# Performance work log

Hardware: AMD Instinct MI355X
Metric: run time of the kernel (lower is better)

Reference implementation:

```python
import jax, jax.numpy as jnp
import numpy as np
import math

EPS = 1e-6
MAX_NORM = 1.0 - 1e-3


def _clip_to_ball(x):
    # Keep point strictly inside the unit ball (||x|| < 1).
    norm = jnp.maximum(jnp.linalg.norm(x, axis=-1, keepdims=True), EPS)
    factor = jnp.minimum(MAX_NORM / norm, 1.0)
    return x * factor


def setup_inputs() -> dict:
    key = jax.random.key(0)
    k1, k2 = jax.random.split(key)
    B, C, D = 8192, 4096, 512
    euclidean_emb = jax.random.normal(k1, (B, D), dtype=jnp.float32)
    centroids = jax.random.uniform(k2, (C, D), dtype=jnp.float32, minval=-0.01, maxval=0.01)
    log_c = jnp.asarray(math.log(1.0), dtype=jnp.float32)
    return {"euclidean_emb": euclidean_emb, "log_c": log_c, "centroids": centroids}


def reference(euclidean_emb, log_c, centroids):
    # torch code used c = self.log_c.exp().item() -> c is detached scalar
    c = jax.lax.stop_gradient(jnp.exp(log_c))
    sqrt_c = jnp.sqrt(c)

    # expmap0: Euclidean -> Poincare ball
    v_norm = jnp.maximum(jnp.linalg.norm(euclidean_emb, axis=-1, keepdims=True), EPS)
    coeff = jnp.tanh(sqrt_c * v_norm) / (sqrt_c * v_norm)
    x_h = _clip_to_ball(coeff * euclidean_emb)   # (B, D)
    cen_h = _clip_to_ball(centroids)             # (C, D)

    # Pairwise Poincare distance via GEMM (same math as the expanded (B,C,D) form):
    # ||x - y||^2 = ||x||^2 + ||y||^2 - 2 <x, y>
    x2_raw = jnp.sum(x_h * x_h, axis=-1)         # (B,)
    y2_raw = jnp.sum(cen_h * cen_h, axis=-1)     # (C,)
    x2 = jnp.minimum(x2_raw, MAX_NORM ** 2)
    y2 = jnp.minimum(y2_raw, MAX_NORM ** 2)
    xy = x_h @ cen_h.T                           # (B, C) GEMM
    diff2 = x2_raw[:, None] + y2_raw[None, :] - 2.0 * xy

    denom = jnp.maximum((1.0 - c * x2)[:, None] * (1.0 - c * y2)[None, :], EPS)
    arg = jnp.maximum(1.0 + c * (2.0 * diff2) / denom, 1.0 + EPS)
    dists = jnp.arccosh(arg) / sqrt_c            # (B, C)
    return dists, x_h, cen_h
```

## Files before the change

### kernel.cpp

```cpp
#include <hip/hip_runtime.h>
#include <math.h>

#define EPSV 1e-6f
#define MAX_NORM (1.0f - 1e-3f)

typedef __attribute__((ext_vector_type(8))) short short8;
typedef __attribute__((ext_vector_type(4))) float f32x4;

__device__ inline ushort f32_to_bf16(float f) {
    union { float f; uint32_t u; } cv;
    cv.f = f;
    uint32_t u = cv.u;
    u += 0x7FFFu + ((u >> 16) & 1u);
    return (ushort)(u >> 16);
}

__device__ inline void glds16(const ushort* gsrc, ushort* ldsdst) {
    auto* g = (const __attribute__((address_space(1))) uint32_t*)gsrc;
    auto* l = (__attribute__((address_space(3))) uint32_t*)ldsdst;
    __builtin_amdgcn_global_load_lds(g, l, 16, 0, 0);
}

__device__ inline short8 ds_read128(const ushort* p) {
    auto* l3 = (const __attribute__((address_space(3))) ushort*)p;
    const uint32_t addr = (uint32_t)(uintptr_t)l3;
    short8 v;
    asm volatile("ds_read_b128 %0, %1" : "=&v"(v) : "v"(addr));
    return v;
}

__global__ void rows_emb_kernel(const float* __restrict__ emb,
                                const float* __restrict__ logc,
                                float* __restrict__ xh,
                                ushort* __restrict__ xbf,
                                float* __restrict__ x2raw,
                                float* __restrict__ dxv) {
    const int D = 512;
    const int row = blockIdx.x;
    const int lane = threadIdx.x;

    const float4* r4 = (const float4*)(emb + (size_t)row * D);
    float4 a = r4[2 * lane];
    float4 b = r4[2 * lane + 1];

    float ss = a.x * a.x + a.y * a.y + a.z * a.z + a.w * a.w
             + b.x * b.x + b.y * b.y + b.z * b.z + b.w * b.w;
#pragma unroll
    for (int off = 32; off > 0; off >>= 1) ss += __shfl_xor(ss, off, 64);

    const float c  = expf(logc[0]);
    const float sc = sqrtf(c);

    const float tn    = sqrtf(ss);
    const float vn    = fmaxf(tn, EPSV);
    const float coeff = tanhf(sc * vn) / (sc * vn);
    const float pre   = coeff * tn;
    const float fac   = fminf(MAX_NORM / fmaxf(pre, EPSV), 1.0f);
    const float scale = coeff * fac;

    float4 oa, ob;
    oa.x = a.x * scale; oa.y = a.y * scale; oa.z = a.z * scale; oa.w = a.w * scale;
    ob.x = b.x * scale; ob.y = b.y * scale; ob.z = b.z * scale; ob.w = b.w * scale;

    float4* o4 = (float4*)(xh + (size_t)row * D);
    o4[2 * lane]     = oa;
    o4[2 * lane + 1] = ob;

    union { ushort u[8]; uint4 v; } pk;
    pk.u[0] = f32_to_bf16(oa.x); pk.u[1] = f32_to_bf16(oa.y);
    pk.u[2] = f32_to_bf16(oa.z); pk.u[3] = f32_to_bf16(oa.w);
    pk.u[4] = f32_to_bf16(ob.x); pk.u[5] = f32_to_bf16(ob.y);
    pk.u[6] = f32_to_bf16(ob.z); pk.u[7] = f32_to_bf16(ob.w);
    ((uint4*)(xbf + (size_t)row * D))[lane] = pk.v;

    if (lane == 0) {
        const float sq = scale * scale * ss;
        x2raw[row] = sq;
        dxv[row]   = 1.0f - c * fminf(sq, MAX_NORM * MAX_NORM);
    }
}

__global__ void rows_cen_kernel(const float* __restrict__ cen,
                                const float* __restrict__ logc,
                                float* __restrict__ ch,
                                ushort* __restrict__ cbf,
                                float* __restrict__ y2raw,
                                float* __restrict__ dyv) {
    const int D = 512;
    const int row = blockIdx.x;
    const int lane = threadIdx.x;

    const float4* r4 = (const float4*)(cen + (size_t)row * D);
    float4 a = r4[2 * lane];
    float4 b = r4[2 * lane + 1];

    float ss = a.x * a.x + a.y * a.y + a.z * a.z + a.w * a.w
             + b.x * b.x + b.y * b.y + b.z * b.z + b.w * b.w;
#pragma unroll
    for (int off = 32; off > 0; off >>= 1) ss += __shfl_xor(ss, off, 64);

    const float c = expf(logc[0]);

    const float tn    = sqrtf(ss);
    const float scale = fminf(MAX_NORM / fmaxf(tn, EPSV), 1.0f);

    float4 oa, ob;
    oa.x = a.x * scale; oa.y = a.y * scale; oa.z = a.z * scale; oa.w = a.w * scale;
    ob.x = b.x * scale; ob.y = b.y * scale; ob.z = b.z * scale; ob.w = b.w * scale;

    float4* o4 = (float4*)(ch + (size_t)row * D);
    o4[2 * lane]     = oa;
    o4[2 * lane + 1] = ob;

    union { ushort u[8]; uint4 v; } pk;
    pk.u[0] = f32_to_bf16(oa.x); pk.u[1] = f32_to_bf16(oa.y);
    pk.u[2] = f32_to_bf16(oa.z); pk.u[3] = f32_to_bf16(oa.w);
    pk.u[4] = f32_to_bf16(ob.x); pk.u[5] = f32_to_bf16(ob.y);
    pk.u[6] = f32_to_bf16(ob.z); pk.u[7] = f32_to_bf16(ob.w);
    ((uint4*)(cbf + (size_t)row * D))[lane] = pk.v;

    if (lane == 0) {
        const float sq = scale * scale * ss;
        y2raw[row] = sq;
        dyv[row]   = 1.0f - c * fminf(sq, MAX_NORM * MAX_NORM);
    }
}

#define BM 256
#define BN 256
#define BKT 32
#define EPST 68

__global__ __launch_bounds__(512, 2)
void gemm_epi_kernel(const ushort* __restrict__ Abf,
                     const ushort* __restrict__ Bbf,
                     const float* __restrict__ x2raw,
                     const float* __restrict__ dxv,
                     const float* __restrict__ y2raw,
                     const float* __restrict__ dyv,
                     const float* __restrict__ logc,
                     float* __restrict__ out,
                     int M, int N, int K) {
    __shared__ __align__(16) char smem[65536];

    const int tid  = threadIdx.x;
    const int lane = tid & 63;
    const int wid  = tid >> 6;
    const int wm   = wid >> 2;
    const int wn   = wid & 3;

    const int bm = blockIdx.y;
    const int bn = blockIdx.x;

    const ushort* Ab = Abf + (size_t)bm * BM * K;
    const ushort* Bb = Bbf + (size_t)bn * BN * K;

    f32x4 acc[8][4];
#pragma unroll
    for (int m = 0; m < 8; m++)
#pragma unroll
        for (int n = 0; n < 4; n++) acc[m][n] = (f32x4){0.f, 0.f, 0.f, 0.f};

    const size_t fragoff = (size_t)(lane & 15) * K + ((lane >> 4) * 8);

    auto Asb = [&](int p) { return (ushort*)(smem + p * 16384); };
    auto Bsb = [&](int p) { return (ushort*)(smem + 32768 + p * 16384); };

    auto stage = [&](int p, int k0) {
#pragma unroll
        for (int j = 0; j < 2; j++) {
            const int s = wid * 2 + j;
            const size_t goff = (size_t)(s * 16) * K + k0 + fragoff;
            glds16(Ab + goff, Asb(p) + s * 512);
            glds16(Bb + goff, Bsb(p) + s * 512);
        }
    };

    stage(0, 0);
    stage(1, BKT);
    asm volatile("s_waitcnt vmcnt(4)" ::: "memory");
    __builtin_amdgcn_s_barrier();

    const int NT = K / BKT;
    int p = 0;
    for (int t = 0; t < NT; t++) {
        short8 af[8], bfr[4];
#pragma unroll
        for (int n = 0; n < 4; n++)
            bfr[n] = ds_read128(Bsb(p) + (wn * 4 + n) * 512 + lane * 8);
        af[0] = ds_read128(Asb(p) + (wm * 8 + 0) * 512 + lane * 8);
        af[1] = ds_read128(Asb(p) + (wm * 8 + 1) * 512 + lane * 8);

#pragma unroll
        for (int q = 0; q < 4; q++) {
            if (q < 3) {
                af[2 * q + 2] = ds_read128(Asb(p) + (wm * 8 + 2 * q + 2) * 512 + lane * 8);
                af[2 * q + 3] = ds_read128(Asb(p) + (wm * 8 + 2 * q + 3) * 512 + lane * 8);
                asm volatile("s_waitcnt lgkmcnt(2)" ::: "memory");
            } else {
                asm volatile("s_waitcnt lgkmcnt(0)" ::: "memory");
            }
            __builtin_amdgcn_sched_barrier(0);
            __builtin_amdgcn_s_setprio(1);
#pragma unroll
            for (int mm = 0; mm < 2; mm++)
#pragma unroll
                for (int n = 0; n < 4; n++)
                    acc[2 * q + mm][n] = __builtin_amdgcn_mfma_f32_16x16x32_bf16(
                        af[2 * q + mm], bfr[n], acc[2 * q + mm][n], 0, 0, 0);
            __builtin_amdgcn_s_setprio(0);
        }

        __builtin_amdgcn_s_barrier();

        if (t + 2 < NT) {
            stage(p, (t + 2) * BKT);
            asm volatile("s_waitcnt vmcnt(4)" ::: "memory");
            __builtin_amdgcn_s_barrier();
        } else if (t + 1 < NT) {
            asm volatile("s_waitcnt vmcnt(0)" ::: "memory");
            __builtin_amdgcn_s_barrier();
        }
        p ^= 1;
    }

    __syncthreads();

    const float c   = expf(logc[0]);
    const float rsc = 1.0f / sqrtf(c);
    const int l16 = lane & 15;
    const int lg  = lane >> 4;

    float* ep = (float*)(smem + (size_t)wid * 4352);
    const int gr_base = bm * BM + wm * 128;
    const int gc_base = bn * BN + wn * 64;

#pragma unroll
    for (int m = 0; m < 8; m++) {
#pragma unroll
        for (int n = 0; n < 4; n++)
#pragma unroll
            for (int r = 0; r < 4; r++)
                ep[(lg * 4 + r) * EPST + n * 16 + l16] = acc[m][n][r];
        asm volatile("s_waitcnt lgkmcnt(0)" ::: "memory");

#pragma unroll
        for (int it = 0; it < 4; it++) {
            const int row = it * 4 + lg;
            const int gr  = gr_base + m * 16 + row;
            const int gc  = gc_base + l16 * 4;
            float4 xy4 = *(const float4*)&ep[row * EPST + l16 * 4];
            const float rx  = x2raw[gr];
            const float dxr = dxv[gr];
            const float4 ry4 = *(const float4*)&y2raw[gc];
            const float4 dy4 = *(const float4*)&dyv[gc];
            float4 o;
            {
                const float rden = __builtin_amdgcn_rcpf(fmaxf(dxr * dy4.x, EPSV));
                float t = fmaxf(2.0f * c * (rx + ry4.x - 2.0f * xy4.x) * rden, EPSV);
                o.x = __logf(1.0f + t + __builtin_amdgcn_sqrtf(t * (t + 2.0f))) * rsc;
            }
            {
                const float rden = __builtin_amdgcn_rcpf(fmaxf(dxr * dy4.y, EPSV));
                float t = fmaxf(2.0f * c * (rx + ry4.y - 2.0f * xy4.y) * rden, EPSV);
                o.y = __logf(1.0f + t + __builtin_amdgcn_sqrtf(t * (t + 2.0f))) * rsc;
            }
            {
                const float rden = __builtin_amdgcn_rcpf(fmaxf(dxr * dy4.z, EPSV));
                float t = fmaxf(2.0f * c * (rx + ry4.z - 2.0f * xy4.z) * rden, EPSV);
                o.z = __logf(1.0f + t + __builtin_amdgcn_sqrtf(t * (t + 2.0f))) * rsc;
            }
            {
                const float rden = __builtin_amdgcn_rcpf(fmaxf(dxr * dy4.w, EPSV));
                float t = fmaxf(2.0f * c * (rx + ry4.w - 2.0f * xy4.w) * rden, EPSV);
                o.w = __logf(1.0f + t + __builtin_amdgcn_sqrtf(t * (t + 2.0f))) * rsc;
            }
            *(float4*)&out[(size_t)gr * N + gc] = o;
        }
        asm volatile("s_waitcnt lgkmcnt(0)" ::: "memory");
    }
}

extern "C" void kernel_launch(void* const* d_in, const int* in_sizes, int n_in,
                              void* d_out, int out_size, void* d_ws, size_t ws_size,
                              hipStream_t stream) {
    const float* emb  = (const float*)d_in[0];
    const float* logc = (const float*)d_in[1];
    const float* cen  = (const float*)d_in[2];

    const int D = 512;
    const int B = in_sizes[0] / D;
    const int C = in_sizes[2] / D;

    float* out   = (float*)d_out;
    float* dists = out;
    float* xh    = out + (size_t)B * C;
    float* ch    = xh + (size_t)B * D;

    char* ws = (char*)d_ws;
    size_t off = 0;
    auto alloc = [&](size_t bytes) -> char* {
        char* p = ws + off;
        off += (bytes + 255) & ~(size_t)255;
        return p;
    };
    ushort* xbf   = (ushort*)alloc((size_t)B * D * sizeof(ushort));
    ushort* cbf   = (ushort*)alloc((size_t)C * D * sizeof(ushort));
    float*  x2raw = (float*)alloc((size_t)B * sizeof(float));
    float*  dxv   = (float*)alloc((size_t)B * sizeof(float));
    float*  y2raw = (float*)alloc((size_t)C * sizeof(float));
    float*  dyv   = (float*)alloc((size_t)C * sizeof(float));

    rows_emb_kernel<<<B, 64, 0, stream>>>(emb, logc, xh, xbf, x2raw, dxv);
    rows_cen_kernel<<<C, 64, 0, stream>>>(cen, logc, ch, cbf, y2raw, dyv);

    dim3 grid(C / BN, B / BM);
    gemm_epi_kernel<<<grid, 512, 0, stream>>>(xbf, cbf, x2raw, dxv, y2raw, dyv,
                                              logc, dists, B, C, D);
}
```

Measured before the change: 88.79 us.

## Use four-stage LDS ring with prefetch depth three and interleaved loads

Replaces the double-buffered LDS staging with a four-buffer ring that prefetches three K-tiles ahead. The global-to-LDS loads for the next tile are now issued inside the MFMA loop, one per sub-step, and each iteration uses a single barrier instead of two. The aim is to hide global load latency better and cut synchronisation. The cost is that shared memory grows to 128 KB per block, which likely stops two blocks from fitting on one CU and removes overlap between blocks.

```diff
diff --git a/kernel.cpp b/kernel.cpp
--- a/kernel.cpp
+++ b/kernel.cpp
@@ -141,7 +141,7 @@
                      const float* __restrict__ logc,
                      float* __restrict__ out,
                      int M, int N, int K) {
-    __shared__ __align__(16) char smem[65536];
+    __shared__ __align__(16) char smem[4 * 32768];
 
     const int tid  = threadIdx.x;
     const int lane = tid & 63;
@@ -163,39 +163,49 @@
 
     const size_t fragoff = (size_t)(lane & 15) * K + ((lane >> 4) * 8);
 
-    auto Asb = [&](int p) { return (ushort*)(smem + p * 16384); };
-    auto Bsb = [&](int p) { return (ushort*)(smem + 32768 + p * 16384); };
-
-    auto stage = [&](int p, int k0) {
-#pragma unroll
-        for (int j = 0; j < 2; j++) {
-            const int s = wid * 2 + j;
-            const size_t goff = (size_t)(s * 16) * K + k0 + fragoff;
-            glds16(Ab + goff, Asb(p) + s * 512);
-            glds16(Bb + goff, Bsb(p) + s * 512);
-        }
+    auto Abuf = [&](int b) { return (ushort*)(smem + b * 32768); };
+    auto Bbuf = [&](int b) { return (ushort*)(smem + b * 32768 + 16384); };
+
+    auto stage_call = [&](int b, int k0, int j) {
+        const int s = wid * 2 + (j & 1);
+        const size_t goff = (size_t)(s * 16) * K + k0 + fragoff;
+        if (j < 2) glds16(Ab + goff, Abuf(b) + s * 512);
+        else       glds16(Bb + goff, Bbuf(b) + s * 512);
     };
 
-    stage(0, 0);
-    stage(1, BKT);
-    asm volatile("s_waitcnt vmcnt(4)" ::: "memory");
-    __builtin_amdgcn_s_barrier();
-
     const int NT = K / BKT;
-    int p = 0;
-    for (int t = 0; t < NT; t++) {
+
+#pragma unroll
+    for (int tt = 0; tt < 3; ++tt)
+#pragma unroll
+        for (int j = 0; j < 4; ++j)
+            stage_call(tt & 3, tt * BKT, j);
+
+    for (int t = 0; t < NT; ++t) {
+        const int b = t & 3;
+
+        if (t <= NT - 3)      asm volatile("s_waitcnt vmcnt(8)" ::: "memory");
+        else if (t == NT - 2) asm volatile("s_waitcnt vmcnt(4)" ::: "memory");
+        else                  asm volatile("s_waitcnt vmcnt(0)" ::: "memory");
+        __builtin_amdgcn_s_barrier();
+
+        const bool do_stage = (t + 3 < NT);
+        const int  sb = (t + 3) & 3;
+        const int  sk = (t + 3) * BKT;
+
         short8 af[8], bfr[4];
 #pragma unroll
         for (int n = 0; n < 4; n++)
-            bfr[n] = ds_read128(Bsb(p) + (wn * 4 + n) * 512 + lane * 8);
-        af[0] = ds_read128(Asb(p) + (wm * 8 + 0) * 512 + lane * 8);
-        af[1] = ds_read128(Asb(p) + (wm * 8 + 1) * 512 + lane * 8);
-
-#pragma unroll
-        for (int q = 0; q < 4; q++) {
+            bfr[n] = ds_read128(Bbuf(b) + (wn * 4 + n) * 512 + lane * 8);
+        af[0] = ds_read128(Abuf(b) + (wm * 8 + 0) * 512 + lane * 8);
+        af[1] = ds_read128(Abuf(b) + (wm * 8 + 1) * 512 + lane * 8);
+
+#pragma unroll
+        for (int q = 0; q < 4; ++q) {
+            if (do_stage) stage_call(sb, sk, q);
             if (q < 3) {
-                af[2 * q + 2] = ds_read128(Asb(p) + (wm * 8 + 2 * q + 2) * 512 + lane * 8);
-                af[2 * q + 3] = ds_read128(Asb(p) + (wm * 8 + 2 * q + 3) * 512 + lane * 8);
+                af[2 * q + 2] = ds_read128(Abuf(b) + (wm * 8 + 2 * q + 2) * 512 + lane * 8);
+                af[2 * q + 3] = ds_read128(Abuf(b) + (wm * 8 + 2 * q + 3) * 512 + lane * 8);
                 asm volatile("s_waitcnt lgkmcnt(2)" ::: "memory");
             } else {
                 asm volatile("s_waitcnt lgkmcnt(0)" ::: "memory");
@@ -210,18 +220,6 @@
                         af[2 * q + mm], bfr[n], acc[2 * q + mm][n], 0, 0, 0);
             __builtin_amdgcn_s_setprio(0);
         }
-
-        __builtin_amdgcn_s_barrier();
-
-        if (t + 2 < NT) {
-            stage(p, (t + 2) * BKT);
-            asm volatile("s_waitcnt vmcnt(4)" ::: "memory");
-            __builtin_amdgcn_s_barrier();
-        } else if (t + 1 < NT) {
-            asm volatile("s_waitcnt vmcnt(0)" ::: "memory");
-            __builtin_amdgcn_s_barrier();
-        }
-        p ^= 1;
     }
 
     __syncthreads();
```

Measured after the change: 86.99 us. 1.02x faster.
